# Performance work log

Hardware: AMD Instinct MI355X
Metric: run time of the kernel (lower is better)

Reference implementation:

```python
import jax, jax.numpy as jnp
import numpy as np
from jax import lax

B, C, T = 8, 512, 4096
K = 3
DILATIONS = (1, 3, 5)
EPS_Q = 1e-5
EPS_SNAKE = 1e-9


def quantize_weight(w):
    # BitNet-1.58-style ternary quantization with per-tensor absmean scale,
    # applied with a straight-through estimator.
    s = jnp.mean(jnp.abs(w))
    wq = jnp.clip(jnp.round(w / (s + EPS_Q)), -1.0, 1.0) * s
    return w + lax.stop_gradient(wq - w)


def bitconv1d(x, w, b, dilation, padding):
    # x: [B, C, T], w: [Cout, Cin, K], b: [Cout]
    y = lax.conv_general_dilated(
        x, quantize_weight(w),
        window_strides=(1,),
        padding=[(padding, padding)],
        rhs_dilation=(dilation,),
        dimension_numbers=("NCH", "OIH", "NCH"),
    )
    return y + b[None, :, None]


def snake_beta(x, alpha_p, beta_p):
    # log-scale parametrization: alpha = exp(alpha_p), beta = exp(beta_p)
    a = jnp.exp(alpha_p)[None, :, None]
    b = jnp.exp(beta_p)[None, :, None]
    return x + (1.0 / (b + EPS_SNAKE)) * jnp.sin(a * x) ** 2


def setup_inputs() -> dict:
    key = jax.random.key(0)
    ks = jax.random.split(key, 7)
    return {
        "x": jax.random.normal(ks[0], (B, C, T), dtype=jnp.float32),
        "w1": jax.random.normal(ks[1], (3, C, C, K), dtype=jnp.float32) * 0.05,
        "b1": jax.random.normal(ks[2], (3, C), dtype=jnp.float32) * 0.01,
        "alpha": jax.random.normal(ks[3], (3, C), dtype=jnp.float32) * 0.1,
        "beta": jax.random.normal(ks[4], (3, C), dtype=jnp.float32) * 0.1,
        "w2": jax.random.normal(ks[5], (3, C, C, K), dtype=jnp.float32) * 0.05,
        "b2": jax.random.normal(ks[6], (3, C), dtype=jnp.float32) * 0.01,
    }


def reference(x, w1, b1, alpha, beta, w2, b2):
    for i, d in enumerate(DILATIONS):
        pad1 = d * (K - 1) // 2
        h = bitconv1d(x, w1[i], b1[i], dilation=d, padding=pad1)
        h = snake_beta(h, alpha[i], beta[i])
        h = bitconv1d(h, w2[i], b2[i], dilation=1, padding=(K - 1) // 2)
        x = x + h
    return x
```

## Files before the change

kernel.cpp:

```cpp
#include <hip/hip_runtime.h>
#include <math.h>
#include <stdint.h>


constexpr int B_ = 8, C_ = 512, T_ = 4096, K_ = 3;
constexpr int WELEM = C_ * C_ * K_;

typedef __bf16 bf16x8 __attribute__((ext_vector_type(8)));
typedef float f32x4 __attribute__((ext_vector_type(4)));
typedef unsigned short u16x8 __attribute__((ext_vector_type(8)));

constexpr size_t OFF_PART = 0;
constexpr size_t OFF_S = 4096;
constexpr size_t OFF_AE = 8192;
constexpr size_t OFF_IB = 16384;
constexpr size_t OFF_WQ1 = 32768;
constexpr size_t OFF_WQ2 = OFF_WQ1 + (size_t)3 * WELEM * 2;
constexpr size_t NBCT = (size_t)B_ * C_ * T_;
constexpr size_t OFF_PHI = OFF_WQ2 + (size_t)3 * WELEM * 2;
constexpr size_t OFF_PLO = OFF_PHI + NBCT * 2;
constexpr size_t OFF_QHI = OFF_PLO + NBCT * 2;
constexpr size_t OFF_QLO = OFF_QHI + NBCT * 2;

__device__ inline unsigned short bf16_rne(float v) {
  unsigned int u = __builtin_bit_cast(unsigned int, v);
  unsigned int r = u + 0x7FFFu + ((u >> 16) & 1u);
  return (unsigned short)(r >> 16);
}

__global__ __launch_bounds__(256)
void absmean_partial(const float* __restrict__ w1, const float* __restrict__ w2,
                     float* __restrict__ part) {
  __shared__ float red[256];
  const int t = blockIdx.y;
  const float* src = (t < 3) ? (w1 + (size_t)t * WELEM) : (w2 + (size_t)(t - 3) * WELEM);
  const int base = blockIdx.x * (256 * 32);
  float v = 0.f;
#pragma unroll
  for (int j = 0; j < 32; ++j) v += fabsf(src[base + j * 256 + threadIdx.x]);
  red[threadIdx.x] = v;
  __syncthreads();
  for (int s = 128; s > 0; s >>= 1) {
    if (threadIdx.x < (unsigned)s) red[threadIdx.x] += red[threadIdx.x + s];
    __syncthreads();
  }
  if (threadIdx.x == 0) part[t * 96 + blockIdx.x] = red[0];
}

__global__ __launch_bounds__(128)
void absmean_final(const float* __restrict__ part, float* __restrict__ svec) {
  __shared__ float red[128];
  const int t = blockIdx.x;
  red[threadIdx.x] = (threadIdx.x < 96) ? part[t * 96 + threadIdx.x] : 0.f;
  __syncthreads();
  for (int s = 64; s > 0; s >>= 1) {
    if (threadIdx.x < (unsigned)s) red[threadIdx.x] += red[threadIdx.x + s];
    __syncthreads();
  }
  if (threadIdx.x == 0) svec[t] = red[0] / (float)WELEM;
}

__global__ __launch_bounds__(256)
void quantize_kernel(const float* __restrict__ src, unsigned short* __restrict__ dst,
                     const float* __restrict__ svec, int sbase) {
  const int idx = blockIdx.x * 256 + threadIdx.x;
  const int j = idx & 7;
  const int lane = (idx >> 3) & 63;
  const int cot = (idx >> 9) & 31;
  const int rest = idx >> 14;
  const int tap = rest % 3;
  const int rest2 = rest / 3;
  const int cc = rest2 & 15;
  const int st = rest2 >> 4;
  const int co = cot * 16 + (lane & 15);
  const int ci = cc * 32 + (lane >> 4) * 8 + j;
  const float s = svec[sbase + st];
  const float w = src[(((size_t)st * C_ + co) * C_ + ci) * K_ + tap];
  float q = rintf(w / (s + 1e-5f));
  q = fminf(1.f, fmaxf(-1.f, q));
  dst[idx] = (unsigned short)(__builtin_bit_cast(unsigned int, q) >> 16);
}

__global__ __launch_bounds__(256)
void snake_params_kernel(const float* __restrict__ al, const float* __restrict__ be,
                         float* __restrict__ ae, float* __restrict__ ib) {
  const int idx = blockIdx.x * 256 + threadIdx.x;
  if (idx < 3 * C_) {
    ae[idx] = expf(al[idx]);
    ib[idx] = 1.f / (expf(be[idx]) + 1e-9f);
  }
}

__global__ __launch_bounds__(256)
void transpose_split(const float* __restrict__ X, unsigned short* __restrict__ Hi,
                     unsigned short* __restrict__ Lo) {
  __shared__ float tile[64][68];
  const int b = blockIdx.z;
  const int c0 = blockIdx.y * 64;
  const int t0 = blockIdx.x * 64;
  const int tid = threadIdx.x;
  {
    const int cl = tid >> 2, tg = tid & 3;
    const float* src = X + ((size_t)b * C_ + c0 + cl) * T_ + t0 + tg * 16;
    float4 v0 = *(const float4*)(src);
    float4 v1 = *(const float4*)(src + 4);
    float4 v2 = *(const float4*)(src + 8);
    float4 v3 = *(const float4*)(src + 12);
    float* d = &tile[cl][tg * 16];
    *(float4*)(d) = v0; *(float4*)(d + 4) = v1;
    *(float4*)(d + 8) = v2; *(float4*)(d + 12) = v3;
  }
  __syncthreads();
  {
    const int tl = tid >> 2, cg = tid & 3;
    u16x8 h0, h1, l0, l1;
#pragma unroll
    for (int j = 0; j < 16; ++j) {
      const float v = tile[cg * 16 + j][tl];
      const unsigned short hb = bf16_rne(v);
      const float hf = __builtin_bit_cast(float, (unsigned int)hb << 16);
      const unsigned short lb = bf16_rne(v - hf);
      if (j < 8) { h0[j] = hb; l0[j] = lb; }
      else       { h1[j - 8] = hb; l1[j - 8] = lb; }
    }
    const size_t off = ((size_t)b * T_ + t0 + tl) * C_ + c0 + cg * 16;
    *(u16x8*)(Hi + off) = h0; *(u16x8*)(Hi + off + 8) = h1;
    *(u16x8*)(Lo + off) = l0; *(u16x8*)(Lo + off + 8) = l1;
  }
}

template <int DIL, bool SNAKE, bool PLANES, bool WF32>
__global__ __launch_bounds__(256, 2)
void conv_mfma(const unsigned short* __restrict__ Xhi,
               const unsigned short* __restrict__ Xlo,
               const unsigned short* __restrict__ Wq,
               const float* __restrict__ svec,
               const float* __restrict__ bias, const float* __restrict__ aexp,
               const float* __restrict__ invb,
               const float* __restrict__ res,
               float* __restrict__ Y,
               unsigned short* __restrict__ Ohi,
               unsigned short* __restrict__ Olo) {
  constexpr int TT = 256;
  constexpr int R = TT + 2 * DIL;
  constexpr int RW = 40;
  __shared__ unsigned short Xs[2][R * RW];

  const int b = blockIdx.z;
  const int co0 = blockIdx.y * 128;
  const int cob = blockIdx.y * 8;
  const int t0 = blockIdx.x * TT;
  const int tid = threadIdx.x;
  const int lane = tid & 63;
  const int wv = tid >> 6;
  const int l15 = lane & 15;
  const int quad = lane >> 4;

  f32x4 acc[8][4] = {};

  const size_t xbase = (size_t)b * T_ * C_;

#pragma unroll 1
  for (int cc = 0; cc < C_ / 32; ++cc) {
    constexpr int XU = R * 8;
#pragma unroll
    for (int it = 0; it < (XU + 255) / 256; ++it) {
      const int u = it * 256 + tid;
      if (u < XU) {
        const int r = u >> 3, sub = u & 7;
        const int pl = sub >> 2, g = sub & 3;
        const int t = t0 - DIL + r;
        u16x8 v = {0, 0, 0, 0, 0, 0, 0, 0};
        if ((unsigned)t < (unsigned)T_)
          v = *(const u16x8*)((pl ? Xlo : Xhi) + xbase + (size_t)t * C_ + cc * 32 + g * 8);
        *(u16x8*)&Xs[pl][r * RW + g * 8] = v;
      }
    }
    __syncthreads();

#pragma unroll 1
    for (int tap = 0; tap < K_; ++tap) {
      const unsigned short* wb =
          Wq + ((((size_t)cc * K_ + tap) * 32 + cob) * 512) + (size_t)lane * 8;
      bf16x8 a[8];
#pragma unroll
      for (int m = 0; m < 8; ++m)
        a[m] = __builtin_bit_cast(bf16x8, *(const u16x8*)(wb + m * 512));
#pragma unroll
      for (int n = 0; n < 4; ++n) {
        const int r = wv * 64 + n * 16 + l15 + tap * DIL;
        const bf16x8 bh = __builtin_bit_cast(bf16x8, *(const u16x8*)&Xs[0][r * RW + quad * 8]);
        const bf16x8 bl = __builtin_bit_cast(bf16x8, *(const u16x8*)&Xs[1][r * RW + quad * 8]);
#pragma unroll
        for (int m = 0; m < 8; ++m) {
          acc[m][n] = __builtin_amdgcn_mfma_f32_16x16x32_bf16(a[m], bh, acc[m][n], 0, 0, 0);
          acc[m][n] = __builtin_amdgcn_mfma_f32_16x16x32_bf16(a[m], bl, acc[m][n], 0, 0, 0);
        }
      }
    }
    __syncthreads();
  }

  const float sw = *svec;

  if (PLANES) {
    uint32_t* E = (uint32_t*)&Xs[0][0];
    constexpr int ELD = 33;
#pragma unroll
    for (int mb = 0; mb < 4; ++mb) {
      __syncthreads();
#pragma unroll
      for (int mm = 0; mm < 2; ++mm) {
        const int m = mb * 2 + mm;
        const int cb = co0 + m * 16 + quad * 4;
        float bs[4], av[4], ibv[4];
#pragma unroll
        for (int reg = 0; reg < 4; ++reg) {
          bs[reg] = bias[cb + reg];
          if (SNAKE) { av[reg] = aexp[cb + reg]; ibv[reg] = invb[cb + reg]; }
        }
#pragma unroll
        for (int n = 0; n < 4; ++n) {
          const int tl = wv * 64 + n * 16 + l15;
          const int t = t0 + tl;
#pragma unroll
          for (int reg = 0; reg < 4; ++reg) {
            float v = sw * acc[m][n][reg] + bs[reg];
            if (SNAKE) {
              const float sn = __sinf(av[reg] * v);
              v = v + ibv[reg] * sn * sn;
            } else {
              v = v + res[((size_t)b * C_ + cb + reg) * T_ + t];
            }
            if (WF32) Y[((size_t)b * C_ + cb + reg) * T_ + t] = v;
            const unsigned short hb = bf16_rne(v);
            const float hf = __builtin_bit_cast(float, (unsigned int)hb << 16);
            const unsigned short lb = bf16_rne(v - hf);
            E[tl * ELD + mm * 16 + quad * 4 + reg] =
                ((unsigned int)hb << 16) | (unsigned int)lb;
          }
        }
      }
      __syncthreads();
      {
        const int row = tid;
        uint32_t u[32];
#pragma unroll
        for (int j = 0; j < 32; ++j) u[j] = E[row * ELD + j];
        u16x8 hq[4], lq[4];
#pragma unroll
        for (int g = 0; g < 4; ++g)
#pragma unroll
          for (int j = 0; j < 8; ++j) {
            hq[g][j] = (unsigned short)(u[g * 8 + j] >> 16);
            lq[g][j] = (unsigned short)(u[g * 8 + j] & 0xFFFFu);
          }
        const size_t poff = ((size_t)b * T_ + t0 + row) * C_ + co0 + mb * 32;
#pragma unroll
        for (int g = 0; g < 4; ++g) {
          *(u16x8*)(Ohi + poff + g * 8) = hq[g];
          *(u16x8*)(Olo + poff + g * 8) = lq[g];
        }
      }
    }
  } else {
#pragma unroll
    for (int m = 0; m < 8; ++m) {
      const int cb = co0 + m * 16 + quad * 4;
      float bs[4], av[4], ibv[4];
#pragma unroll
      for (int reg = 0; reg < 4; ++reg) {
        bs[reg] = bias[cb + reg];
        if (SNAKE) { av[reg] = aexp[cb + reg]; ibv[reg] = invb[cb + reg]; }
      }
#pragma unroll
      for (int n = 0; n < 4; ++n) {
        const int t = t0 + wv * 64 + n * 16 + l15;
#pragma unroll
        for (int reg = 0; reg < 4; ++reg) {
          float v = sw * acc[m][n][reg] + bs[reg];
          if (SNAKE) {
            const float sn = __sinf(av[reg] * v);
            v = v + ibv[reg] * sn * sn;
          } else {
            v = v + res[((size_t)b * C_ + cb + reg) * T_ + t];
          }
          Y[((size_t)b * C_ + cb + reg) * T_ + t] = v;
        }
      }
    }
  }
}

extern "C" void kernel_launch(void* const* d_in, const int* in_sizes, int n_in,
                              void* d_out, int out_size, void* d_ws, size_t ws_size,
                              hipStream_t stream) {
  (void)in_sizes; (void)n_in; (void)out_size; (void)ws_size;
  const float* x = (const float*)d_in[0];
  const float* w1 = (const float*)d_in[1];
  const float* b1 = (const float*)d_in[2];
  const float* al = (const float*)d_in[3];
  const float* be = (const float*)d_in[4];
  const float* w2 = (const float*)d_in[5];
  const float* b2 = (const float*)d_in[6];
  float* out = (float*)d_out;
  char* wsb = (char*)d_ws;

  float* part = (float*)(wsb + OFF_PART);
  float* svec = (float*)(wsb + OFF_S);
  float* ae = (float*)(wsb + OFF_AE);
  float* ib = (float*)(wsb + OFF_IB);
  unsigned short* wq1 = (unsigned short*)(wsb + OFF_WQ1);
  unsigned short* wq2 = (unsigned short*)(wsb + OFF_WQ2);
  unsigned short* Phi = (unsigned short*)(wsb + OFF_PHI);
  unsigned short* Plo = (unsigned short*)(wsb + OFF_PLO);
  unsigned short* Qhi = (unsigned short*)(wsb + OFF_QHI);
  unsigned short* Qlo = (unsigned short*)(wsb + OFF_QLO);

  absmean_partial<<<dim3(96, 6), 256, 0, stream>>>(w1, w2, part);
  absmean_final<<<6, 128, 0, stream>>>(part, svec);
  quantize_kernel<<<(3 * WELEM) / 256, 256, 0, stream>>>(w1, wq1, svec, 0);
  quantize_kernel<<<(3 * WELEM) / 256, 256, 0, stream>>>(w2, wq2, svec, 3);
  snake_params_kernel<<<6, 256, 0, stream>>>(al, be, ae, ib);

  const dim3 tgrid(T_ / 64, C_ / 64, B_);
  const dim3 cgrid(T_ / 256, C_ / 128, B_);

  transpose_split<<<tgrid, 256, 0, stream>>>(x, Phi, Plo);

  conv_mfma<1, true, true, false><<<cgrid, 256, 0, stream>>>(
      Phi, Plo, wq1 + 0 * (size_t)WELEM, svec + 0, b1 + 0, ae + 0, ib + 0,
      nullptr, nullptr, Qhi, Qlo);
  conv_mfma<1, false, true, true><<<cgrid, 256, 0, stream>>>(
      Qhi, Qlo, wq2 + 0 * (size_t)WELEM, svec + 3, b2 + 0, nullptr, nullptr,
      x, out, Phi, Plo);

  conv_mfma<3, true, true, false><<<cgrid, 256, 0, stream>>>(
      Phi, Plo, wq1 + 1 * (size_t)WELEM, svec + 1, b1 + C_, ae + C_, ib + C_,
      nullptr, nullptr, Qhi, Qlo);
  conv_mfma<1, false, true, true><<<cgrid, 256, 0, stream>>>(
      Qhi, Qlo, wq2 + 1 * (size_t)WELEM, svec + 4, b2 + C_, nullptr, nullptr,
      out, out, Phi, Plo);

  conv_mfma<5, true, true, false><<<cgrid, 256, 0, stream>>>(
      Phi, Plo, wq1 + 2 * (size_t)WELEM, svec + 2, b1 + 2 * C_, ae + 2 * C_,
      ib + 2 * C_, nullptr, nullptr, Qhi, Qlo);
  conv_mfma<1, false, false, true><<<cgrid, 256, 0, stream>>>(
      Qhi, Qlo, wq2 + 2 * (size_t)WELEM, svec + 5, b2 + 2 * C_, nullptr, nullptr,
      out, out, nullptr, nullptr);
}
```

Before: 842.3 us.

## Double-buffer conv input tiles via async global_load_lds with XOR-swizzled LDS

```diff
diff --git a/kernel.cpp b/kernel.cpp
--- a/kernel.cpp
+++ b/kernel.cpp
@@ -21,6 +21,7 @@
 constexpr size_t OFF_PLO = OFF_PHI + NBCT * 2;
 constexpr size_t OFF_QHI = OFF_PLO + NBCT * 2;
 constexpr size_t OFF_QLO = OFF_QHI + NBCT * 2;
+constexpr size_t OFF_ZERO = OFF_QLO + NBCT * 2;
 
 __device__ inline unsigned short bf16_rne(float v) {
   unsigned int u = __builtin_bit_cast(unsigned int, v);
@@ -83,12 +84,14 @@
 
 __global__ __launch_bounds__(256)
 void snake_params_kernel(const float* __restrict__ al, const float* __restrict__ be,
-                         float* __restrict__ ae, float* __restrict__ ib) {
+                         float* __restrict__ ae, float* __restrict__ ib,
+                         float* __restrict__ zr) {
   const int idx = blockIdx.x * 256 + threadIdx.x;
   if (idx < 3 * C_) {
     ae[idx] = expf(al[idx]);
     ib[idx] = 1.f / (expf(be[idx]) + 1e-9f);
   }
+  if (idx < 1024) zr[idx] = 0.f;
 }
 
 __global__ __launch_bounds__(256)
@@ -134,6 +137,7 @@
 void conv_mfma(const unsigned short* __restrict__ Xhi,
                const unsigned short* __restrict__ Xlo,
                const unsigned short* __restrict__ Wq,
+               unsigned int zoff,
                const float* __restrict__ svec,
                const float* __restrict__ bias, const float* __restrict__ aexp,
                const float* __restrict__ invb,
@@ -143,8 +147,10 @@
                unsigned short* __restrict__ Olo) {
   constexpr int TT = 256;
   constexpr int R = TT + 2 * DIL;
-  constexpr int RW = 40;
-  __shared__ unsigned short Xs[2][R * RW];
+  constexpr int R8 = (R + 7) & ~7;
+  constexpr int W8 = R8 / 8;
+  constexpr int NW = (W8 + 3) / 4;
+  __shared__ unsigned short Xs[2][R8 * 64];
 
   const int b = blockIdx.z;
   const int co0 = blockIdx.y * 128;
@@ -159,29 +165,76 @@
   f32x4 acc[8][4] = {};
 
   const size_t xbase = (size_t)b * T_ * C_;
+  const unsigned int plo_delta = (unsigned int)(NBCT * 2);
+  const char* xh8 = (const char*)Xhi;
+
+  unsigned int offs[NW];
+#pragma unroll
+  for (int j = 0; j < NW; ++j) {
+    const int wnd = wv + j * 4;
+    const int rl = wnd * 8 + (lane >> 3);
+    const int cpr = (lane & 7) ^ (rl & 7);
+    const int p = cpr >> 2, g = cpr & 3;
+    const int t = t0 - DIL + rl;
+    unsigned int o;
+    if (wnd < W8 && (unsigned)t < (unsigned)T_)
+      o = (p ? plo_delta : 0u) + (unsigned int)((xbase + (size_t)t * C_ + g * 8) * 2);
+    else
+      o = zoff + (unsigned int)(g * 16);
+    offs[j] = o;
+  }
+
+  auto stage = [&](int cc, int buf) {
+#pragma unroll
+    for (int j = 0; j < NW; ++j) {
+      const int wnd = wv + j * 4;
+      if (wnd < W8) {
+        const char* gp = xh8 + offs[j] + cc * 64;
+        __builtin_amdgcn_global_load_lds(
+            (const __attribute__((address_space(1))) unsigned int*)gp,
+            (__attribute__((address_space(3))) unsigned int*)&Xs[buf][wnd * 512],
+            16, 0, 0);
+      }
+    }
+  };
+
+  stage(0, 0);
+  __syncthreads();
 
 #pragma unroll 1
   for (int cc = 0; cc < C_ / 32; ++cc) {
-    constexpr int XU = R * 8;
-#pragma unroll
-    for (int it = 0; it < (XU + 255) / 256; ++it) {
-      const int u = it * 256 + tid;
-      if (u < XU) {
-        const int r = u >> 3, sub = u & 7;
-        const int pl = sub >> 2, g = sub & 3;
-        const int t = t0 - DIL + r;
-        u16x8 v = {0, 0, 0, 0, 0, 0, 0, 0};
-        if ((unsigned)t < (unsigned)T_)
-          v = *(const u16x8*)((pl ? Xlo : Xhi) + xbase + (size_t)t * C_ + cc * 32 + g * 8);
-        *(u16x8*)&Xs[pl][r * RW + g * 8] = v;
-      }
-    }
-    __syncthreads();
-
-#pragma unroll 1
-    for (int tap = 0; tap < K_; ++tap) {
+    const int cur = cc & 1;
+
+    bf16x8 a0[8];
+    {
       const unsigned short* wb =
-          Wq + ((((size_t)cc * K_ + tap) * 32 + cob) * 512) + (size_t)lane * 8;
+          Wq + (((size_t)cc * K_ + 0) * 32 + cob) * 512 + (size_t)lane * 8;
+#pragma unroll
+      for (int m = 0; m < 8; ++m)
+        a0[m] = __builtin_bit_cast(bf16x8, *(const u16x8*)(wb + m * 512));
+    }
+
+    if (cc < C_ / 32 - 1) stage(cc + 1, 1 - cur);
+
+#pragma unroll
+    for (int n = 0; n < 4; ++n) {
+      const int r = wv * 64 + n * 16 + l15;
+      const int rw = (r & 7) * 8;
+      const bf16x8 bh =
+          __builtin_bit_cast(bf16x8, *(const u16x8*)&Xs[cur][r * 64 + ((quad * 8) ^ rw)]);
+      const bf16x8 bl =
+          __builtin_bit_cast(bf16x8, *(const u16x8*)&Xs[cur][r * 64 + ((quad * 8 + 32) ^ rw)]);
+#pragma unroll
+      for (int m = 0; m < 8; ++m) {
+        acc[m][n] = __builtin_amdgcn_mfma_f32_16x16x32_bf16(a0[m], bh, acc[m][n], 0, 0, 0);
+        acc[m][n] = __builtin_amdgcn_mfma_f32_16x16x32_bf16(a0[m], bl, acc[m][n], 0, 0, 0);
+      }
+    }
+
+#pragma unroll
+    for (int tap = 1; tap < K_; ++tap) {
+      const unsigned short* wb =
+          Wq + (((size_t)cc * K_ + tap) * 32 + cob) * 512 + (size_t)lane * 8;
       bf16x8 a[8];
 #pragma unroll
       for (int m = 0; m < 8; ++m)
@@ -189,8 +242,11 @@
 #pragma unroll
       for (int n = 0; n < 4; ++n) {
         const int r = wv * 64 + n * 16 + l15 + tap * DIL;
-        const bf16x8 bh = __builtin_bit_cast(bf16x8, *(const u16x8*)&Xs[0][r * RW + quad * 8]);
-        const bf16x8 bl = __builtin_bit_cast(bf16x8, *(const u16x8*)&Xs[1][r * RW + quad * 8]);
+        const int rw = (r & 7) * 8;
+        const bf16x8 bh =
+            __builtin_bit_cast(bf16x8, *(const u16x8*)&Xs[cur][r * 64 + ((quad * 8) ^ rw)]);
+        const bf16x8 bl =
+            __builtin_bit_cast(bf16x8, *(const u16x8*)&Xs[cur][r * 64 + ((quad * 8 + 32) ^ rw)]);
 #pragma unroll
         for (int m = 0; m < 8; ++m) {
           acc[m][n] = __builtin_amdgcn_mfma_f32_16x16x32_bf16(a[m], bh, acc[m][n], 0, 0, 0);
@@ -316,12 +372,16 @@
   unsigned short* Plo = (unsigned short*)(wsb + OFF_PLO);
   unsigned short* Qhi = (unsigned short*)(wsb + OFF_QHI);
   unsigned short* Qlo = (unsigned short*)(wsb + OFF_QLO);
+  float* zr = (float*)(wsb + OFF_ZERO);
+
+  const unsigned int zoffP = (unsigned int)(OFF_ZERO - OFF_PHI);
+  const unsigned int zoffQ = (unsigned int)(OFF_ZERO - OFF_QHI);
 
   absmean_partial<<<dim3(96, 6), 256, 0, stream>>>(w1, w2, part);
   absmean_final<<<6, 128, 0, stream>>>(part, svec);
   quantize_kernel<<<(3 * WELEM) / 256, 256, 0, stream>>>(w1, wq1, svec, 0);
   quantize_kernel<<<(3 * WELEM) / 256, 256, 0, stream>>>(w2, wq2, svec, 3);
-  snake_params_kernel<<<6, 256, 0, stream>>>(al, be, ae, ib);
+  snake_params_kernel<<<6, 256, 0, stream>>>(al, be, ae, ib, zr);
 
   const dim3 tgrid(T_ / 64, C_ / 64, B_);
   const dim3 cgrid(T_ / 256, C_ / 128, B_);
@@ -329,23 +389,23 @@
   transpose_split<<<tgrid, 256, 0, stream>>>(x, Phi, Plo);
 
   conv_mfma<1, true, true, false><<<cgrid, 256, 0, stream>>>(
-      Phi, Plo, wq1 + 0 * (size_t)WELEM, svec + 0, b1 + 0, ae + 0, ib + 0,
+      Phi, Plo, wq1 + 0 * (size_t)WELEM, zoffP, svec + 0, b1 + 0, ae + 0, ib + 0,
       nullptr, nullptr, Qhi, Qlo);
   conv_mfma<1, false, true, true><<<cgrid, 256, 0, stream>>>(
-      Qhi, Qlo, wq2 + 0 * (size_t)WELEM, svec + 3, b2 + 0, nullptr, nullptr,
+      Qhi, Qlo, wq2 + 0 * (size_t)WELEM, zoffQ, svec + 3, b2 + 0, nullptr, nullptr,
       x, out, Phi, Plo);
 
   conv_mfma<3, true, true, false><<<cgrid, 256, 0, stream>>>(
-      Phi, Plo, wq1 + 1 * (size_t)WELEM, svec + 1, b1 + C_, ae + C_, ib + C_,
+      Phi, Plo, wq1 + 1 * (size_t)WELEM, zoffP, svec + 1, b1 + C_, ae + C_, ib + C_,
       nullptr, nullptr, Qhi, Qlo);
   conv_mfma<1, false, true, true><<<cgrid, 256, 0, stream>>>(
-      Qhi, Qlo, wq2 + 1 * (size_t)WELEM, svec + 4, b2 + C_, nullptr, nullptr,
+      Qhi, Qlo, wq2 + 1 * (size_t)WELEM, zoffQ, svec + 4, b2 + C_, nullptr, nullptr,
       out, out, Phi, Plo);
 
   conv_mfma<5, true, true, false><<<cgrid, 256, 0, stream>>>(
-      Phi, Plo, wq1 + 2 * (size_t)WELEM, svec + 2, b1 + 2 * C_, ae + 2 * C_,
+      Phi, Plo, wq1 + 2 * (size_t)WELEM, zoffP, svec + 2, b1 + 2 * C_, ae + 2 * C_,
       ib + 2 * C_, nullptr, nullptr, Qhi, Qlo);
   conv_mfma<1, false, false, true><<<cgrid, 256, 0, stream>>>(
-      Qhi, Qlo, wq2 + 2 * (size_t)WELEM, svec + 5, b2 + 2 * C_, nullptr, nullptr,
+      Qhi, Qlo, wq2 + 2 * (size_t)WELEM, zoffQ, svec + 5, b2 + 2 * C_, nullptr, nullptr,
       out, out, nullptr, nullptr);
 }
```

Measured after the change: 751.1 us. -10.8%, faster.
